# Kernel tuning notes

Hardware: AMD Instinct MI355X
Metric: run time of the kernel (lower is better)

The kernel has to match this reference:

```python
import jax, jax.numpy as jnp
import numpy as np

SMOOTH = 9.0   # self.labmda
EPS = 1e-8
MASK_VAL = -1.0

I, R, D = 64, 36, 1024   # n_image, n_regions, d
C, W = 64, 32            # n_caption, max_n_word


def setup_inputs() -> dict:
    key = jax.random.key(0)
    k1, k2, k3, k4 = jax.random.split(key, 4)
    imgs = jax.random.normal(k1, (I, R, D), dtype=jnp.float32)
    caps = jax.random.normal(k2, (C, W, D), dtype=jnp.float32)
    img_lens = jax.random.randint(k3, (I,), 1, R + 1)
    cap_lens = jnp.maximum(jax.random.randint(k4, (C,), 0, W + 1), 4)
    return {"imgs": imgs, "caps": caps, "img_lens": img_lens, "cap_lens": cap_lens}


def reference(imgs, caps, img_lens, cap_lens):
    # imgs: (I,R,D) images/regions; caps: (C,W,D); cap_lens: (C,)
    # Vectorized over captions: padded word positions are masked so the
    # per-caption word-dim l2norm matches the ragged torch loop exactly.
    wmask = jnp.arange(W)[None, :] < cap_lens[:, None]          # (C,W)
    wmask_f = wmask.astype(imgs.dtype)

    # attn[c,i,w,r] = <caps[c,w], imgs[i,r]>  (torch: bmm(context, queryT))
    attn = jnp.einsum('ird,cwd->ciwr', imgs, caps)              # (C,I,W,R)
    attn = jax.nn.leaky_relu(attn, 0.1)
    attn = attn * wmask_f[:, None, :, None]                     # zero padded words
    # l2norm over word dim (torch l2norm(attn, 2) on (I,R,W)): eps after sqrt
    norm_w = jnp.sqrt(jnp.sum(attn * attn, axis=2, keepdims=True)) + EPS
    attn = attn / norm_w
    # temperature-scaled softmax over regions
    attn = jax.nn.softmax(attn * SMOOTH, axis=3)                # (C,I,W,R)

    # weighted context per word, l2-normalized over feature dim
    wctx = jnp.einsum('ciwr,ird->ciwd', attn, imgs)             # (C,I,W,D)
    wctx = wctx / (jnp.sqrt(jnp.sum(wctx * wctx, axis=-1, keepdims=True)) + EPS)

    # cosine similarity between the word and its attended context
    cap_e = caps[:, None, :, :]                                 # (C,1,W,D)
    w12 = jnp.sum(cap_e * wctx, axis=-1)                        # (C,I,W)
    w1 = jnp.sqrt(jnp.sum(cap_e * cap_e, axis=-1))
    w2 = jnp.sqrt(jnp.sum(wctx * wctx, axis=-1))
    sim = w12 / jnp.maximum(w1 * w2, EPS)                       # (C,I,W)

    sim = jnp.where(wmask[:, None, :], sim, MASK_VAL)
    return jnp.transpose(sim, (1, 0, 2))                        # (I,C,W)
```

## Files before the change

### kernel.cpp

```cpp
#include <hip/hip_runtime.h>
#include <hip/hip_bf16.h>

#define IDIM 64
#define RDIM 36
#define DDIM 1024
#define CDIM 64
#define WDIM 32
#define SMOOTH 9.0f
#define EPSF 1e-8f

typedef __bf16 bf16_t;
typedef __bf16 bf16x8 __attribute__((ext_vector_type(8)));
typedef __bf16 bf16x4 __attribute__((ext_vector_type(4)));
typedef float f32x4 __attribute__((ext_vector_type(4)));

#define MFMA16(a, b, c) __builtin_amdgcn_mfma_f32_16x16x32_bf16((a), (b), (c), 0, 0, 0)

#define IMGSB_OFF 0
#define IMGSB_BYTES (IDIM * 4 * 8 * 3 * 512 * 2)
#define CAPSA_OFF (IMGSB_OFF + IMGSB_BYTES)
#define CAPSA_BYTES (CDIM * 4 * 8 * 2 * 512 * 2)
#define GF_OFF    (CAPSA_OFF + CAPSA_BYTES)
#define GF_BYTES  (IDIM * 384 * 8 * 2)
#define CAPN_OFF  (GF_OFF + GF_BYTES)

__global__ __launch_bounds__(256) void prep_kernel(
    const float* __restrict__ imgs, const float* __restrict__ caps,
    bf16_t* __restrict__ imgsB, bf16_t* __restrict__ capsA) {
  __shared__ __align__(16) bf16_t ldsb[36 * 264];
  int b = blockIdx.x, tid = threadIdx.x;
  if (b < 256) {
    int i = b >> 2, wvk = b & 3, ks = wvk * 256;
    const float* src = imgs + (size_t)i * RDIM * DDIM + ks;
#pragma unroll
    for (int rep = 0; rep < 9; ++rep) {
      int idx = rep * 256 + tid;
      int row = idx >> 6, q = idx & 63;
      float4 v = *(const float4*)(src + (size_t)row * DDIM + q * 4);
      bf16x4 p;
      p[0] = (bf16_t)v.x; p[1] = (bf16_t)v.y; p[2] = (bf16_t)v.z; p[3] = (bf16_t)v.w;
      *(bf16x4*)&ldsb[row * 264 + q * 4] = p;
    }
    __syncthreads();
    bf16_t* dst = imgsB + (size_t)(i * 4 + wvk) * 12288;
#pragma unroll
    for (int rep = 0; rep < 6; ++rep) {
      int u = rep * 256 + tid;
      int kk = u / 192, rem = u - kk * 192;
      int nt = rem >> 6, lane = rem & 63, qd = lane >> 4, l15 = lane & 15;
      int row = nt * 16 + l15;
      bf16x8 p;
      if (row < 36) {
        p = *(const bf16x8*)&ldsb[row * 264 + kk * 32 + qd * 8];
      } else {
#pragma unroll
        for (int j = 0; j < 8; ++j) p[j] = (bf16_t)0.0f;
      }
      *(bf16x8*)(dst + (size_t)u * 8) = p;
    }
  } else {
    int bb = b - 256;
    int c = bb >> 2, wvk = bb & 3, ks = wvk * 256;
    const float* src = caps + (size_t)c * WDIM * DDIM + ks;
#pragma unroll
    for (int rep = 0; rep < 8; ++rep) {
      int idx = rep * 256 + tid;
      int row = idx >> 6, q = idx & 63;
      float4 v = *(const float4*)(src + (size_t)row * DDIM + q * 4);
      bf16x4 p;
      p[0] = (bf16_t)v.x; p[1] = (bf16_t)v.y; p[2] = (bf16_t)v.z; p[3] = (bf16_t)v.w;
      *(bf16x4*)&ldsb[row * 264 + q * 4] = p;
    }
    __syncthreads();
    bf16_t* dst = capsA + (size_t)(c * 4 + wvk) * 8192;
#pragma unroll
    for (int rep = 0; rep < 4; ++rep) {
      int u = rep * 256 + tid;
      int kk = u >> 7, rem = u & 127;
      int mt = rem >> 6, lane = rem & 63, qd = lane >> 4, l15 = lane & 15;
      int row = mt * 16 + l15;
      bf16x8 p = *(const bf16x8*)&ldsb[row * 264 + kk * 32 + qd * 8];
      *(bf16x8*)(dst + (size_t)u * 8) = p;
    }
  }
}

__global__ __launch_bounds__(256) void gram_kernel(
    const bf16_t* __restrict__ imgsB, const bf16_t* __restrict__ capsA,
    bf16_t* __restrict__ Gfrag, float* __restrict__ capnorm) {
  __shared__ float part[4][48][49];
  __shared__ float cnl[4][32];
  int bx = blockIdx.x;
  int tid = threadIdx.x, wv = tid >> 6, ln = tid & 63;
  int l15 = ln & 15, qd = ln >> 4;
  if (bx < 64) {
    int i = bx;
    const bf16_t* base = imgsB + (size_t)(i * 4 + wv) * 12288;
    f32x4 acc[3][3];
#pragma unroll
    for (int mt = 0; mt < 3; ++mt)
#pragma unroll
      for (int nt = 0; nt < 3; ++nt) {
        f32x4 zf = {0.f, 0.f, 0.f, 0.f};
        acc[mt][nt] = zf;
      }
#pragma unroll
    for (int kk = 0; kk < 8; ++kk) {
      bf16x8 a[3];
#pragma unroll
      for (int nt = 0; nt < 3; ++nt)
        a[nt] = *(const bf16x8*)(base + ((size_t)(kk * 3 + nt) * 64 + ln) * 8);
#pragma unroll
      for (int mt = 0; mt < 3; ++mt)
#pragma unroll
        for (int nt = 0; nt < 3; ++nt)
          acc[mt][nt] = MFMA16(a[mt], a[nt], acc[mt][nt]);
    }
#pragma unroll
    for (int mt = 0; mt < 3; ++mt)
#pragma unroll
      for (int nt = 0; nt < 3; ++nt)
#pragma unroll
        for (int rg = 0; rg < 4; ++rg)
          part[wv][mt * 16 + qd * 4 + rg][nt * 16 + l15] = acc[mt][nt][rg];
    __syncthreads();
    for (int idx = tid; idx < 384; idx += 256) {
      int kk = idx / 192;
      int rem = idx - kk * 192;
      int nt = rem >> 6, lnn = rem & 63;
      int qd2 = lnn >> 4, l152 = lnn & 15;
      int n = nt * 16 + l152;
      bf16x8 pk;
#pragma unroll
      for (int j = 0; j < 8; ++j) {
        int k = kk * 32 + qd2 * 8 + j;
        float v = (k < 48) ? (part[0][k][n] + part[1][k][n] + part[2][k][n] + part[3][k][n]) : 0.f;
        pk[j] = (bf16_t)v;
      }
      *(bf16x8*)(Gfrag + ((size_t)i * 384 + idx) * 8) = pk;
    }
  } else {
    int c = bx - 64;
    const bf16_t* base = capsA + (size_t)(c * 4 + wv) * 8192;
    float ss0 = 0.f, ss1 = 0.f;
#pragma unroll
    for (int kk = 0; kk < 8; ++kk) {
      bf16x8 p0 = *(const bf16x8*)(base + ((size_t)(kk * 2 + 0) * 64 + ln) * 8);
      bf16x8 p1 = *(const bf16x8*)(base + ((size_t)(kk * 2 + 1) * 64 + ln) * 8);
#pragma unroll
      for (int j = 0; j < 8; ++j) {
        float v0 = (float)p0[j], v1 = (float)p1[j];
        ss0 += v0 * v0;
        ss1 += v1 * v1;
      }
    }
    ss0 += __shfl_xor(ss0, 16, 64); ss0 += __shfl_xor(ss0, 32, 64);
    ss1 += __shfl_xor(ss1, 16, 64); ss1 += __shfl_xor(ss1, 32, 64);
    if (qd == 0) { cnl[wv][l15] = ss0; cnl[wv][16 + l15] = ss1; }
    __syncthreads();
    if (tid < 32)
      capnorm[c * 32 + tid] = sqrtf(cnl[0][tid] + cnl[1][tid] + cnl[2][tid] + cnl[3][tid]);
  }
}

__global__ __launch_bounds__(256, 4) void main_kernel(
    const bf16_t* __restrict__ capsA, const bf16_t* __restrict__ imgsB,
    const bf16_t* __restrict__ Gfrag, const float* __restrict__ capnorm,
    const int* __restrict__ cap_lens, float* __restrict__ out) {
  __shared__ __align__(16) bf16_t ldsB[2][6144];

  int bx = blockIdx.x;
  int wv = threadIdx.x >> 6, ln = threadIdx.x & 63;
  int l15 = ln & 15, qd = ln >> 4;
  int xcd = bx & 7, rest = bx >> 3;
  int ih = rest & 7, cq = rest >> 3;
  int i = xcd * 8 + ih;
  int c = cq * 4 + wv;
  int clen = cap_lens[c];

  const bf16_t* Ab = capsA + (size_t)c * 32768;
  const bf16_t* Bb = imgsB + (size_t)i * 49152;

  bf16x8 t0, t1, t2;
  {
    const bf16_t* gp = Bb + wv * 1536 + ln * 8;
    t0 = *(const bf16x8*)(gp);
    t1 = *(const bf16x8*)(gp + 512);
    t2 = *(const bf16x8*)(gp + 1024);
    bf16_t* lp = &ldsB[0][wv * 1536 + ln * 8];
    *(bf16x8*)(lp) = t0;
    *(bf16x8*)(lp + 512) = t1;
    *(bf16x8*)(lp + 1024) = t2;
  }
  __syncthreads();

  f32x4 acc[2][3];
#pragma unroll
  for (int mt = 0; mt < 2; ++mt)
#pragma unroll
    for (int nt = 0; nt < 3; ++nt) {
      f32x4 zf = {0.f, 0.f, 0.f, 0.f};
      acc[mt][nt] = zf;
    }

  for (int ch = 0; ch < 8; ++ch) {
    int p = ch & 1;
    if (ch < 7) {
      const bf16_t* gp = Bb + (ch + 1) * 6144 + wv * 1536 + ln * 8;
      t0 = *(const bf16x8*)(gp);
      t1 = *(const bf16x8*)(gp + 512);
      t2 = *(const bf16x8*)(gp + 1024);
    }
#pragma unroll
    for (int j = 0; j < 4; ++j) {
      int s = ch * 4 + j;
      const bf16_t* ap = Ab + (size_t)s * 1024 + ln * 8;
      bf16x8 a0 = *(const bf16x8*)(ap);
      bf16x8 a1 = *(const bf16x8*)(ap + 512);
      const bf16_t* lp = &ldsB[p][j * 1536 + ln * 8];
      bf16x8 b0 = *(const bf16x8*)(lp);
      bf16x8 b1 = *(const bf16x8*)(lp + 512);
      bf16x8 b2 = *(const bf16x8*)(lp + 1024);
      acc[0][0] = MFMA16(a0, b0, acc[0][0]);
      acc[0][1] = MFMA16(a0, b1, acc[0][1]);
      acc[0][2] = MFMA16(a0, b2, acc[0][2]);
      acc[1][0] = MFMA16(a1, b0, acc[1][0]);
      acc[1][1] = MFMA16(a1, b1, acc[1][1]);
      acc[1][2] = MFMA16(a1, b2, acc[1][2]);
    }
    if (ch < 7) {
      bf16_t* lp = &ldsB[1 - p][wv * 1536 + ln * 8];
      *(bf16x8*)(lp) = t0;
      *(bf16x8*)(lp + 512) = t1;
      *(bf16x8*)(lp + 1024) = t2;
    }
    __syncthreads();
  }

  const bf16_t* Gb = Gfrag + (size_t)i * 3072;
  bf16x8 ga[2][3];
#pragma unroll
  for (int kk = 0; kk < 2; ++kk)
#pragma unroll
    for (int nt = 0; nt < 3; ++nt)
      ga[kk][nt] = *(const bf16x8*)(Gb + ((size_t)(kk * 3 + nt) * 64 + ln) * 8);

  float sinv[3];
#pragma unroll
  for (int nt = 0; nt < 3; ++nt) {
    bool padn = (nt == 2) && (l15 >= 4);
    float ns = 0.f;
#pragma unroll
    for (int mt = 0; mt < 2; ++mt)
#pragma unroll
      for (int rg = 0; rg < 4; ++rg) {
        float v = acc[mt][nt][rg];
        float l = (v > 0.f) ? v : 0.1f * v;
        int m = mt * 16 + qd * 4 + rg;
        if (m >= clen || padn) l = 0.f;
        ns += l * l;
      }
    ns += __shfl_xor(ns, 16, 64);
    ns += __shfl_xor(ns, 32, 64);
    sinv[nt] = SMOOTH / (sqrtf(ns) + EPSF);
  }

  float Srow[2][4];
#pragma unroll
  for (int mt = 0; mt < 2; ++mt)
#pragma unroll
    for (int rg = 0; rg < 4; ++rg) {
      int m = mt * 16 + qd * 4 + rg;
      bool mrow = (m >= clen);
      float z[3];
#pragma unroll
      for (int nt = 0; nt < 3; ++nt) {
        float v = acc[mt][nt][rg];
        float l = (v > 0.f) ? v : 0.1f * v;
        if (mrow) l = 0.f;
        float zz = l * sinv[nt];
        if (nt == 2 && l15 >= 4) zz = -1e30f;
        z[nt] = zz;
      }
      float mx = fmaxf(fmaxf(z[0], z[1]), z[2]);
#pragma unroll
      for (int off = 1; off < 16; off <<= 1) mx = fmaxf(mx, __shfl_xor(mx, off, 64));
      float e[3], es = 0.f;
#pragma unroll
      for (int nt = 0; nt < 3; ++nt) {
        e[nt] = __expf(z[nt] - mx);
        es += e[nt];
      }
#pragma unroll
      for (int off = 1; off < 16; off <<= 1) es += __shfl_xor(es, off, 64);
      float inv = 1.0f / es;
      float sac = 0.f;
#pragma unroll
      for (int nt = 0; nt < 3; ++nt) {
        float a = e[nt] * inv;
        sac += a * acc[mt][nt][rg];
        acc[mt][nt][rg] = a;
      }
#pragma unroll
      for (int off = 1; off < 16; off <<= 1) sac += __shfl_xor(sac, off, 64);
      Srow[mt][rg] = sac;
    }

  bf16_t* as = &ldsB[0][0] + wv * 2304;
#pragma unroll
  for (int mt = 0; mt < 2; ++mt)
#pragma unroll
    for (int nt = 0; nt < 3; ++nt)
#pragma unroll
      for (int rg = 0; rg < 4; ++rg)
        as[(mt * 16 + qd * 4 + rg) * 72 + nt * 16 + l15] = (bf16_t)acc[mt][nt][rg];
  {
    bf16x8 z8;
#pragma unroll
    for (int q = 0; q < 8; ++q) z8[q] = (bf16_t)0.0f;
    *(bf16x8*)(as + (ln >> 1) * 72 + 48 + (ln & 1) * 8) = z8;
  }
  bf16x8 fa[2][2];
#pragma unroll
  for (int mt = 0; mt < 2; ++mt)
#pragma unroll
    for (int kk = 0; kk < 2; ++kk)
      fa[mt][kk] = *(const bf16x8*)(as + (mt * 16 + l15) * 72 + kk * 32 + qd * 8);

  f32x4 y[2][3];
#pragma unroll
  for (int mt = 0; mt < 2; ++mt)
#pragma unroll
    for (int nt = 0; nt < 3; ++nt) {
      f32x4 zf = {0.f, 0.f, 0.f, 0.f};
      y[mt][nt] = zf;
    }
#pragma unroll
  for (int kk = 0; kk < 2; ++kk)
#pragma unroll
    for (int mt = 0; mt < 2; ++mt)
#pragma unroll
      for (int nt = 0; nt < 3; ++nt)
        y[mt][nt] = MFMA16(fa[mt][kk], ga[kk][nt], y[mt][nt]);

  float n2row[2][4];
#pragma unroll
  for (int mt = 0; mt < 2; ++mt)
#pragma unroll
    for (int rg = 0; rg < 4; ++rg) {
      float nn = 0.f;
#pragma unroll
      for (int nt = 0; nt < 3; ++nt) nn += y[mt][nt][rg] * acc[mt][nt][rg];
#pragma unroll
      for (int off = 1; off < 16; off <<= 1) nn += __shfl_xor(nn, off, 64);
      n2row[mt][rg] = nn;
    }

  if (l15 < 2) {
    int mt = l15;
    f32x4 cn = *(const f32x4*)(capnorm + c * 32 + mt * 16 + qd * 4);
    f32x4 o;
#pragma unroll
    for (int rg = 0; rg < 4; ++rg) {
      float n2v = fmaxf(n2row[mt][rg], 0.f);
      float nrm = sqrtf(n2v);
      float den = nrm + EPSF;
      float w12 = Srow[mt][rg] / den;
      float w2 = nrm / den;
      float sim = w12 / fmaxf(cn[rg] * w2, EPSF);
      int m = mt * 16 + qd * 4 + rg;
      if (m >= clen) sim = -1.0f;
      o[rg] = sim;
    }
    *(f32x4*)(out + ((size_t)i * CDIM + c) * WDIM + mt * 16 + qd * 4) = o;
  }
}

extern "C" void kernel_launch(void* const* d_in, const int* in_sizes, int n_in,
                              void* d_out, int out_size, void* d_ws, size_t ws_size,
                              hipStream_t stream) {
  const float* imgs = (const float*)d_in[0];
  const float* caps = (const float*)d_in[1];
  const int* cap_lens = (const int*)d_in[3];
  float* out = (float*)d_out;

  char* ws = (char*)d_ws;
  bf16_t* imgsB = (bf16_t*)(ws + IMGSB_OFF);
  bf16_t* capsA = (bf16_t*)(ws + CAPSA_OFF);
  bf16_t* Gfrag = (bf16_t*)(ws + GF_OFF);
  float* capnorm = (float*)(ws + CAPN_OFF);

  prep_kernel<<<512, 256, 0, stream>>>(imgs, caps, imgsB, capsA);
  gram_kernel<<<128, 256, 0, stream>>>(imgsB, capsA, Gfrag, capnorm);
  main_kernel<<<1024, 256, 0, stream>>>(capsA, imgsB, Gfrag, capnorm, cap_lens, out);
}
```

Before: 100.7 us.

## Fuse prep and gram kernels into one launch with LDS-resident fragments

Merges the bf16 conversion/fragment packing kernel and the Gram/caption-norm kernel into a single kernel of 128 blocks. Each block now loops over all four K-chunks itself, keeps the image fragments in LDS for the Gram MFMAs, and computes caption norms from the fp32 inputs while converting. This removes a launch and the global re-read of packed data, but cuts the grid from 512 to 128 blocks and uses large LDS (about 135 KB per block), so the preprocessing runs with far less parallelism. Caption norms now come from fp32 values rather than bf16-rounded ones.

```diff
diff --git a/kernel.cpp b/kernel.cpp
--- a/kernel.cpp
+++ b/kernel.cpp
@@ -24,78 +24,52 @@
 #define GF_BYTES  (IDIM * 384 * 8 * 2)
 #define CAPN_OFF  (GF_OFF + GF_BYTES)
 
-__global__ __launch_bounds__(256) void prep_kernel(
+__global__ __launch_bounds__(256) void prep_fused(
     const float* __restrict__ imgs, const float* __restrict__ caps,
-    bf16_t* __restrict__ imgsB, bf16_t* __restrict__ capsA) {
-  __shared__ __align__(16) bf16_t ldsb[36 * 264];
+    bf16_t* __restrict__ imgsB, bf16_t* __restrict__ capsA,
+    bf16_t* __restrict__ Gfrag, float* __restrict__ capnorm) {
+  __shared__ __align__(16) char smem0[4 * 48 * 49 * 4];
+  __shared__ __align__(16) bf16_t fragL[4][12288];
+  bf16_t* ldsb = (bf16_t*)smem0;
+  float (*part)[48][49] = (float(*)[48][49])smem0;
+
   int b = blockIdx.x, tid = threadIdx.x;
-  if (b < 256) {
-    int i = b >> 2, wvk = b & 3, ks = wvk * 256;
-    const float* src = imgs + (size_t)i * RDIM * DDIM + ks;
-#pragma unroll
-    for (int rep = 0; rep < 9; ++rep) {
-      int idx = rep * 256 + tid;
-      int row = idx >> 6, q = idx & 63;
-      float4 v = *(const float4*)(src + (size_t)row * DDIM + q * 4);
-      bf16x4 p;
-      p[0] = (bf16_t)v.x; p[1] = (bf16_t)v.y; p[2] = (bf16_t)v.z; p[3] = (bf16_t)v.w;
-      *(bf16x4*)&ldsb[row * 264 + q * 4] = p;
-    }
-    __syncthreads();
-    bf16_t* dst = imgsB + (size_t)(i * 4 + wvk) * 12288;
-#pragma unroll
-    for (int rep = 0; rep < 6; ++rep) {
-      int u = rep * 256 + tid;
-      int kk = u / 192, rem = u - kk * 192;
-      int nt = rem >> 6, lane = rem & 63, qd = lane >> 4, l15 = lane & 15;
-      int row = nt * 16 + l15;
-      bf16x8 p;
-      if (row < 36) {
-        p = *(const bf16x8*)&ldsb[row * 264 + kk * 32 + qd * 8];
-      } else {
-#pragma unroll
-        for (int j = 0; j < 8; ++j) p[j] = (bf16_t)0.0f;
-      }
-      *(bf16x8*)(dst + (size_t)u * 8) = p;
-    }
-  } else {
-    int bb = b - 256;
-    int c = bb >> 2, wvk = bb & 3, ks = wvk * 256;
-    const float* src = caps + (size_t)c * WDIM * DDIM + ks;
-#pragma unroll
-    for (int rep = 0; rep < 8; ++rep) {
-      int idx = rep * 256 + tid;
-      int row = idx >> 6, q = idx & 63;
-      float4 v = *(const float4*)(src + (size_t)row * DDIM + q * 4);
-      bf16x4 p;
-      p[0] = (bf16_t)v.x; p[1] = (bf16_t)v.y; p[2] = (bf16_t)v.z; p[3] = (bf16_t)v.w;
-      *(bf16x4*)&ldsb[row * 264 + q * 4] = p;
-    }
-    __syncthreads();
-    bf16_t* dst = capsA + (size_t)(c * 4 + wvk) * 8192;
-#pragma unroll
-    for (int rep = 0; rep < 4; ++rep) {
-      int u = rep * 256 + tid;
-      int kk = u >> 7, rem = u & 127;
-      int mt = rem >> 6, lane = rem & 63, qd = lane >> 4, l15 = lane & 15;
-      int row = mt * 16 + l15;
-      bf16x8 p = *(const bf16x8*)&ldsb[row * 264 + kk * 32 + qd * 8];
-      *(bf16x8*)(dst + (size_t)u * 8) = p;
-    }
-  }
-}
-
-__global__ __launch_bounds__(256) void gram_kernel(
-    const bf16_t* __restrict__ imgsB, const bf16_t* __restrict__ capsA,
-    bf16_t* __restrict__ Gfrag, float* __restrict__ capnorm) {
-  __shared__ float part[4][48][49];
-  __shared__ float cnl[4][32];
-  int bx = blockIdx.x;
-  int tid = threadIdx.x, wv = tid >> 6, ln = tid & 63;
+  int wv = tid >> 6, ln = tid & 63;
   int l15 = ln & 15, qd = ln >> 4;
-  if (bx < 64) {
-    int i = bx;
-    const bf16_t* base = imgsB + (size_t)(i * 4 + wv) * 12288;
+
+  if (b < 64) {
+    int i = b;
+    for (int wvk = 0; wvk < 4; ++wvk) {
+      const float* src = imgs + (size_t)i * RDIM * DDIM + wvk * 256;
+#pragma unroll
+      for (int rep = 0; rep < 9; ++rep) {
+        int idx = rep * 256 + tid;
+        int row = idx >> 6, q = idx & 63;
+        float4 v = *(const float4*)(src + (size_t)row * DDIM + q * 4);
+        bf16x4 p;
+        p[0] = (bf16_t)v.x; p[1] = (bf16_t)v.y; p[2] = (bf16_t)v.z; p[3] = (bf16_t)v.w;
+        *(bf16x4*)&ldsb[row * 264 + q * 4] = p;
+      }
+      __syncthreads();
+      bf16_t* dst = imgsB + (size_t)(i * 4 + wvk) * 12288;
+#pragma unroll
+      for (int rep = 0; rep < 6; ++rep) {
+        int u = rep * 256 + tid;
+        int kk = u / 192, rem = u - kk * 192;
+        int nt = rem >> 6, lane = rem & 63, qd2 = lane >> 4, l152 = lane & 15;
+        int row = nt * 16 + l152;
+        bf16x8 p;
+        if (row < 36) {
+          p = *(const bf16x8*)&ldsb[row * 264 + kk * 32 + qd2 * 8];
+        } else {
+#pragma unroll
+          for (int j = 0; j < 8; ++j) p[j] = (bf16_t)0.0f;
+        }
+        *(bf16x8*)(dst + (size_t)u * 8) = p;
+        *(bf16x8*)&fragL[wvk][u * 8] = p;
+      }
+      __syncthreads();
+    }
     f32x4 acc[3][3];
 #pragma unroll
     for (int mt = 0; mt < 3; ++mt)
@@ -109,7 +83,7 @@
       bf16x8 a[3];
 #pragma unroll
       for (int nt = 0; nt < 3; ++nt)
-        a[nt] = *(const bf16x8*)(base + ((size_t)(kk * 3 + nt) * 64 + ln) * 8);
+        a[nt] = *(const bf16x8*)&fragL[wv][((kk * 3 + nt) * 64 + ln) * 8];
 #pragma unroll
       for (int mt = 0; mt < 3; ++mt)
 #pragma unroll
@@ -140,26 +114,42 @@
       *(bf16x8*)(Gfrag + ((size_t)i * 384 + idx) * 8) = pk;
     }
   } else {
-    int c = bx - 64;
-    const bf16_t* base = capsA + (size_t)(c * 4 + wv) * 8192;
-    float ss0 = 0.f, ss1 = 0.f;
-#pragma unroll
-    for (int kk = 0; kk < 8; ++kk) {
-      bf16x8 p0 = *(const bf16x8*)(base + ((size_t)(kk * 2 + 0) * 64 + ln) * 8);
-      bf16x8 p1 = *(const bf16x8*)(base + ((size_t)(kk * 2 + 1) * 64 + ln) * 8);
-#pragma unroll
-      for (int j = 0; j < 8; ++j) {
-        float v0 = (float)p0[j], v1 = (float)p1[j];
-        ss0 += v0 * v0;
-        ss1 += v1 * v1;
-      }
-    }
-    ss0 += __shfl_xor(ss0, 16, 64); ss0 += __shfl_xor(ss0, 32, 64);
-    ss1 += __shfl_xor(ss1, 16, 64); ss1 += __shfl_xor(ss1, 32, 64);
-    if (qd == 0) { cnl[wv][l15] = ss0; cnl[wv][16 + l15] = ss1; }
-    __syncthreads();
-    if (tid < 32)
-      capnorm[c * 32 + tid] = sqrtf(cnl[0][tid] + cnl[1][tid] + cnl[2][tid] + cnl[3][tid]);
+    int c = b - 64;
+    const float* src = caps + (size_t)c * WDIM * DDIM;
+    float ss[8];
+#pragma unroll
+    for (int rep = 0; rep < 8; ++rep) ss[rep] = 0.f;
+    for (int wvk = 0; wvk < 4; ++wvk) {
+#pragma unroll
+      for (int rep = 0; rep < 8; ++rep) {
+        int idx = rep * 256 + tid;
+        int row = idx >> 6, q = idx & 63;
+        float4 v = *(const float4*)(src + (size_t)row * DDIM + wvk * 256 + q * 4);
+        ss[rep] += v.x * v.x + v.y * v.y + v.z * v.z + v.w * v.w;
+        bf16x4 p;
+        p[0] = (bf16_t)v.x; p[1] = (bf16_t)v.y; p[2] = (bf16_t)v.z; p[3] = (bf16_t)v.w;
+        *(bf16x4*)&ldsb[row * 264 + q * 4] = p;
+      }
+      __syncthreads();
+      bf16_t* dst = capsA + (size_t)(c * 4 + wvk) * 8192;
+#pragma unroll
+      for (int rep = 0; rep < 4; ++rep) {
+        int u = rep * 256 + tid;
+        int kk = u >> 7, rem = u & 127;
+        int mt = rem >> 6, lane = rem & 63, qd2 = lane >> 4, l152 = lane & 15;
+        int row = mt * 16 + l152;
+        bf16x8 p = *(const bf16x8*)&ldsb[row * 264 + kk * 32 + qd2 * 8];
+        *(bf16x8*)(dst + (size_t)u * 8) = p;
+      }
+      __syncthreads();
+    }
+#pragma unroll
+    for (int rep = 0; rep < 8; ++rep) {
+      float s = ss[rep];
+#pragma unroll
+      for (int off = 32; off >= 1; off >>= 1) s += __shfl_xor(s, off, 64);
+      if (ln == rep) capnorm[c * 32 + rep * 4 + wv] = sqrtf(s);
+    }
   }
 }
 
@@ -390,7 +380,6 @@
   bf16_t* Gfrag = (bf16_t*)(ws + GF_OFF);
   float* capnorm = (float*)(ws + CAPN_OFF);
 
-  prep_kernel<<<512, 256, 0, stream>>>(imgs, caps, imgsB, capsA);
-  gram_kernel<<<128, 256, 0, stream>>>(imgsB, capsA, Gfrag, capnorm);
+  prep_fused<<<128, 256, 0, stream>>>(imgs, caps, imgsB, capsA, Gfrag, capnorm);
   main_kernel<<<1024, 256, 0, stream>>>(capsA, imgsB, Gfrag, capnorm, cap_lens, out);
 }
```

Result: faster. 98.56 us, median of 2 (-2.1%).
